# Kernel optimization log

Measured on AMD Instinct MI355X. Metric: run time of the kernel, lower is better.

## Reference

```python
import jax, jax.numpy as jnp
import numpy as np

B, N, D, H, PSI = 8, 7225, 256, 8, 64
DH = D // H
DF = 4 * D
EPS = 1e-5


def _ln(x, g, b):
    m = jnp.mean(x, axis=-1, keepdims=True)
    v = jnp.mean((x - m) ** 2, axis=-1, keepdims=True)
    return (x - m) / jnp.sqrt(v + EPS) * g + b


def _gelu(x):
    return jax.nn.gelu(x, approximate=False)


def setup_inputs() -> dict:
    key = jax.random.key(0)
    ks = jax.random.split(key, 16)
    w = lambda k, s: (jax.random.normal(k, s, dtype=jnp.float32) * 0.02)
    inp = {
        'x': jax.random.normal(ks[0], (B, N, D), dtype=jnp.float32),
        'fx': jax.random.normal(ks[1], (B, N, D), dtype=jnp.float32),
        'ln1_g': jnp.ones((D,), jnp.float32), 'ln1_b': jnp.zeros((D,), jnp.float32),
        'Wq': w(ks[2], (D, D)), 'Wk': w(ks[3], (D, D)), 'Wv': w(ks[4], (D, D)),
        'Wo': w(ks[5], (D, D)), 'bo': jnp.zeros((D,), jnp.float32),
        'ln2_g': jnp.ones((D,), jnp.float32), 'ln2_b': jnp.zeros((D,), jnp.float32),
        'mlp_W1': w(ks[6], (D, DF)), 'mlp_b1': jnp.zeros((DF,), jnp.float32),
        'mlp_W2': w(ks[7], (DF, D)), 'mlp_b2': jnp.zeros((D,), jnp.float32),
        'proj_W1': w(ks[8], (D, D)), 'proj_b1': jnp.zeros((D,), jnp.float32),
        'proj_W2': w(ks[9], (D, PSI)), 'proj_b2': jnp.zeros((PSI,), jnp.float32),
        'mu': jnp.zeros((PSI,), jnp.float32),
        'ln3_g': jnp.ones((D,), jnp.float32), 'ln3_b': jnp.zeros((D,), jnp.float32),
        'mlp2_W1': w(ks[10], (D, DF)), 'mlp2_b1': jnp.zeros((DF,), jnp.float32),
        'mlp2_W2': w(ks[11], (DF, D)), 'mlp2_b2': jnp.zeros((D,), jnp.float32),
    }
    return inp


def _forward(x, fx, ln1_g, ln1_b, Wq, Wk, Wv, Wo, bo, ln2_g, ln2_b,
             mlp_W1, mlp_b1, mlp_W2, mlp_b2, proj_W1, proj_b1, proj_W2, proj_b2,
             mu, ln3_g, ln3_b, mlp2_W1, mlp2_b1, mlp2_W2, mlp2_b2):
    # --- linear (kernelized, non-causal) self-attention ---
    h = _ln(x, ln1_g, ln1_b)
    to_heads = lambda t: t.reshape(B, N, H, DH).transpose(0, 2, 1, 3)  # bhnd
    q = to_heads(h @ Wq)
    k = to_heads(h @ Wk)
    v = to_heads(h @ Wv)
    q = jax.nn.softmax(q, axis=-1) * (DH ** -0.5)   # feature-dim softmax
    k = jax.nn.softmax(k, axis=-2)                  # sequence-dim softmax
    ctx = jnp.einsum('bhnd,bhne->bhde', k, v)       # [B,H,DH,DH]
    attn = jnp.einsum('bhnd,bhde->bhne', q, ctx)    # [B,H,N,DH]
    attn = attn.transpose(0, 2, 1, 3).reshape(B, N, D) @ Wo + bo
    x = attn + x

    # --- MLP block (n_layers=0, no residual inside MLP) ---
    h = _ln(x, ln2_g, ln2_b)
    x = _gelu(h @ mlp_W1 + mlp_b1) @ mlp_W2 + mlp_b2 + x

    # --- low-rank projection + covariance whitening (orth=True, training path) ---
    x_ = _gelu(x @ proj_W1 + proj_b1) @ proj_W2 + proj_b2       # [B,N,PSI]
    cov = jnp.einsum('blc,bld->cd', x_, x_) / (B * N)           # [PSI,PSI]
    L = jnp.linalg.cholesky(cov)
    L_inv_T = jnp.linalg.inv(L).T
    x_ = x_ @ L_inv_T

    # --- softplus-scaled low-rank operator on fx ---
    ctx2 = jnp.einsum('blp,bld->bpd', x_, fx)                   # [B,PSI,D]
    fx = jnp.einsum('blp,bpd->bld', x_ * jax.nn.softplus(mu), ctx2)

    fx = _gelu(_ln(fx, ln3_g, ln3_b) @ mlp2_W1 + mlp2_b1) @ mlp2_W2 + mlp2_b2
    return x, fx


def reference(x, fx, ln1_g, ln1_b, Wq, Wk, Wv, Wo, bo, ln2_g, ln2_b,
              mlp_W1, mlp_b1, mlp_W2, mlp_b2, proj_W1, proj_b1, proj_W2, proj_b2,
              mu, ln3_g, ln3_b, mlp2_W1, mlp2_b1, mlp2_W2, mlp2_b2):
    return _forward(x, fx, ln1_g, ln1_b, Wq, Wk, Wv, Wo, bo, ln2_g, ln2_b,
                    mlp_W1, mlp_b1, mlp_W2, mlp_b2, proj_W1, proj_b1, proj_W2, proj_b2,
                    mu, ln3_g, ln3_b, mlp2_W1, mlp2_b1, mlp2_W2, mlp2_b2)
```

## Files before the change

kernel.cpp:

```cpp
#include <hip/hip_runtime.h>
#include <math.h>

typedef unsigned short u16;
typedef unsigned int u32;
typedef float f32x4 __attribute__((ext_vector_type(4)));
typedef __bf16 bf16x8 __attribute__((ext_vector_type(8)));

#define NTOK 57800
#define NSEQ 7225
#define NBATCH 8

static __device__ __forceinline__ float bf2f(u16 u){ u32 x=((u32)u)<<16; float f; __builtin_memcpy(&f,&x,4); return f; }
static __device__ __forceinline__ u16 f2bf(float f){ u32 x; __builtin_memcpy(&x,&f,4); u32 r=x+0x7fffu+((x>>16)&1u); return (u16)(r>>16); }
static __device__ __forceinline__ float gelu_f(float v){
  float y = 0.7978845608028654f * v * (1.0f + 0.044715f * v * v);
  float ay = fabsf(y);
  float e = __expf(-2.0f * ay);
  float th = (1.0f - e) / (1.0f + e);
  th = (y < 0.f) ? -th : th;
  return 0.5f * v * (1.0f + th);
}

static __device__ __forceinline__ void gl16(const u16* g, u16* l){
  __builtin_amdgcn_global_load_lds((const __attribute__((address_space(1))) void*)g,
                                   (__attribute__((address_space(3))) void*)l, 16, 0, 0);
}

struct WJobs { const float* src[10]; u16* dst[10]; int K[10]; int N[10]; };
__global__ __launch_bounds__(256) void wtrans_all(WJobs j){
  int z = blockIdx.z;
  int K = j.K[z], N = j.N[z];
  int bk = blockIdx.x*32, bn = blockIdx.y*32;
  if (bk >= K || bn >= N) return;
  const float* src = j.src[z];
  u16* dst = j.dst[z];
  __shared__ float t[32][33];
  int tx = threadIdx.x&31, ty = threadIdx.x>>5;
  #pragma unroll
  for (int u=0;u<4;u++){
    int k = bk+ty+u*8, n = bn+tx;
    if (k<K && n<N) t[ty+u*8][tx] = src[(long)k*N+n];
  }
  __syncthreads();
  #pragma unroll
  for (int u=0;u<4;u++){
    int n = bn+ty+u*8, k = bk+tx;
    if (n<N && k<K) dst[(long)n*K+k] = f2bf(t[tx][ty+u*8]);
  }
}

__global__ __launch_bounds__(256) void ln_kernel(const float* __restrict__ in, const float* __restrict__ g,
                                                 const float* __restrict__ b, u16* __restrict__ out, int rows){
  int wid = threadIdx.x>>6, lane = threadIdx.x&63;
  int row = blockIdx.x*4 + wid;
  if (row >= rows) return;
  const float4 xv = *reinterpret_cast<const float4*>(in + (long)row*256 + lane*4);
  float s = xv.x+xv.y+xv.z+xv.w;
  float s2 = xv.x*xv.x+xv.y*xv.y+xv.z*xv.z+xv.w*xv.w;
  #pragma unroll
  for (int o=32;o;o>>=1){ s += __shfl_xor(s,o,64); s2 += __shfl_xor(s2,o,64); }
  float mean = s*(1.f/256.f);
  float var = fmaxf(s2*(1.f/256.f) - mean*mean, 0.f);
  float rstd = rsqrtf(var + 1e-5f);
  float4 gv = *reinterpret_cast<const float4*>(g + lane*4);
  float4 bv = *reinterpret_cast<const float4*>(b + lane*4);
  ushort4 o4;
  o4.x = f2bf((xv.x-mean)*rstd*gv.x + bv.x);
  o4.y = f2bf((xv.y-mean)*rstd*gv.y + bv.y);
  o4.z = f2bf((xv.z-mean)*rstd*gv.z + bv.z);
  o4.w = f2bf((xv.w-mean)*rstd*gv.w + bv.w);
  *reinterpret_cast<ushort4*>(out + (long)row*256 + lane*4) = o4;
}

template<bool BIASF, bool RESF, bool GELUF, bool OF32, bool OBF16>
__global__ __launch_bounds__(256) void gemm3(const u16* __restrict__ A, const u16* __restrict__ Bt,
    const float* __restrict__ bias, const float* __restrict__ resid,
    float* __restrict__ outF, u16* __restrict__ outB,
    int M, int N, int K, int gn, long aB, long bB, long cB)
{
  __shared__ __align__(16) u16 lds[2][8192];
  int nwg = gridDim.x, bid = blockIdx.x;
  int qx = nwg>>3, rx = nwg&7;
  int xcd = bid&7, lin = bid>>3;
  int swz = (xcd<rx)? (xcd*(qx+1)+lin) : (rx + xcd*qx + lin);
  int mi_ = swz/gn;
  int m0 = mi_*128, n0 = (swz - mi_*gn)*128;

  const u16* Ab  = A  + (long)blockIdx.z*aB;
  const u16* Btb = Bt + (long)blockIdx.z*bB;
  long coff = (long)blockIdx.z*cB;
  int tid = threadIdx.x, w = tid>>6, l = tid&63;
  int lr = l>>3;
  int csrc = (((l&7) ^ lr) << 3);
  int l15 = l&15, lq = l>>4;
  int wm = (w>>1)*64, wn = (w&1)*64;
  int sx = (l15&7)<<3;

  f32x4 acc[4][4];
  #pragma unroll
  for (int a=0;a<4;a++)
    #pragma unroll
    for (int b2=0;b2<4;b2++)
      #pragma unroll
      for (int r2=0;r2<4;r2++) acc[a][b2][r2]=0.f;

  int nt = K>>6;

  auto STAGE = [&](int k0){
    #pragma unroll
    for (int u=0;u<4;u++){
      int rr = w*32 + u*8;
      gl16(Ab  + (long)(m0+rr+lr)*K + k0 + csrc, &lds[0][0] + rr*64 + l*8);
      gl16(Btb + (long)(n0+rr+lr)*K + k0 + csrc, &lds[1][0] + rr*64 + l*8);
    }
  };

  STAGE(0);
  for (int t=0;;t++){
    __syncthreads();
    #pragma unroll
    for (int ks=0;ks<2;ks++){
      bf16x8 af[4], bfv[4];
      int ko = ks*32 + lq*8;
      #pragma unroll
      for (int mi=0;mi<4;mi++)
        af[mi]  = *reinterpret_cast<const bf16x8*>(&lds[0][0] + (wm+mi*16+l15)*64 + (ko ^ sx));
      #pragma unroll
      for (int ni=0;ni<4;ni++)
        bfv[ni] = *reinterpret_cast<const bf16x8*>(&lds[1][0] + (wn+ni*16+l15)*64 + (ko ^ sx));
      #pragma unroll
      for (int mi=0;mi<4;mi++)
        #pragma unroll
        for (int ni=0;ni<4;ni++)
          acc[mi][ni] = __builtin_amdgcn_mfma_f32_16x16x32_bf16(bfv[ni], af[mi], acc[mi][ni], 0,0,0);
    }
    if (t+1 == nt) break;
    __syncthreads();
    STAGE((t+1)<<6);
  }

  #pragma unroll
  for (int mi=0;mi<4;mi++){
    int row = m0 + wm + mi*16 + l15;
    if (row >= M) continue;
    #pragma unroll
    for (int ni=0;ni<4;ni++){
      int col0 = n0 + wn + ni*16 + lq*4;
      if (col0 >= N) continue;
      f32x4 v = acc[mi][ni];
      if (BIASF){
        const float4 bv = *reinterpret_cast<const float4*>(bias + col0);
        v[0]+=bv.x; v[1]+=bv.y; v[2]+=bv.z; v[3]+=bv.w;
      }
      long idx = (long)row*N + col0;
      if (RESF){
        const float4 rv = *reinterpret_cast<const float4*>(resid + coff + idx);
        v[0]+=rv.x; v[1]+=rv.y; v[2]+=rv.z; v[3]+=rv.w;
      }
      if (GELUF){
        #pragma unroll
        for (int r2=0;r2<4;r2++) v[r2] = gelu_f(v[r2]);
      }
      if (OF32){
        float4 o; o.x=v[0]; o.y=v[1]; o.z=v[2]; o.w=v[3];
        *reinterpret_cast<float4*>(outF + coff + idx) = o;
      }
      if (OBF16){
        ushort4 o; o.x=f2bf(v[0]); o.y=f2bf(v[1]); o.z=f2bf(v[2]); o.w=f2bf(v[3]);
        *reinterpret_cast<ushort4*>(outB + coff + idx) = o;
      }
    }
  }
}

__global__ __launch_bounds__(256) void ctx_part(const u16* __restrict__ qkvb, float* __restrict__ part,
                                                float* __restrict__ spart2){
  int ch = blockIdx.x, bh = blockIdx.y; int b = bh>>3, h = bh&7;
  __shared__ float ek[8][32], vl[8][32];
  int tid = threadIdx.x;
  int d = tid&31, eg = (tid>>5)*4;
  float acc[4] = {0.f,0.f,0.f,0.f};
  float ssum = 0.f;
  int n0 = ch*226; int n1 = n0+226; if (n1 > NSEQ) n1 = NSEQ;
  for (int nb=n0; nb<n1; nb+=8){
    #pragma unroll
    for (int u=0;u<2;u++){
      int idx = tid + u*256; int r = idx>>6, c = idx&63;
      int n = nb + r;
      if (c < 32) ek[r][c]    = (n<n1)? __expf(bf2f(qkvb[((long)(b*NSEQ+n))*768 + 256 + h*32 + c])) : 0.f;
      else        vl[r][c-32] = (n<n1)? bf2f(qkvb[((long)(b*NSEQ+n))*768 + 512 + h*32 + (c-32)]) : 0.f;
    }
    __syncthreads();
    #pragma unroll
    for (int r=0;r<8;r++){
      float kv = ek[r][d];
      ssum += kv;
      #pragma unroll
      for (int j=0;j<4;j++) acc[j] += kv * vl[r][eg+j];
    }
    __syncthreads();
  }
  #pragma unroll
  for (int j=0;j<4;j++) part[((long)(bh*32+ch))*1024 + d*32 + eg + j] = acc[j];
  if (tid < 32) spart2[(bh*32+ch)*32 + d] = ssum;
}
__global__ void ctx_red(const float* __restrict__ part, const float* __restrict__ spart2,
                        float* __restrict__ ctx){
  int bh = blockIdx.x;
  __shared__ float sinvl[32];
  int tid = threadIdx.x;
  if (tid < 32){
    float s=0.f;
    for (int ch=0;ch<32;ch++) s += spart2[(bh*32+ch)*32 + tid];
    sinvl[tid] = 1.0f/s;
  }
  __syncthreads();
  for (int idx=tid; idx<1024; idx+=256){
    float s=0.f;
    for (int ch=0;ch<32;ch++) s += part[((long)(bh*32+ch))*1024 + idx];
    ctx[(long)bh*1024 + idx] = s * sinvl[idx>>5];
  }
}

__global__ __launch_bounds__(256) void qsoftmax(const u16* __restrict__ qkvb, u16* __restrict__ qsb){
  int wid = threadIdx.x>>6, lane = threadIdx.x&63;
  int n = blockIdx.x*4 + wid;
  int b = blockIdx.y;
  if (n >= NSEQ) return;
  const ushort4 qv = *reinterpret_cast<const ushort4*>(qkvb + ((long)(b*NSEQ+n))*768 + lane*4);
  float e0 = __expf(bf2f(qv.x)), e1 = __expf(bf2f(qv.y)),
        e2 = __expf(bf2f(qv.z)), e3 = __expf(bf2f(qv.w));
  float s = e0+e1+e2+e3;
  s += __shfl_xor(s,1,64); s += __shfl_xor(s,2,64); s += __shfl_xor(s,4,64);
  float r = 0.17677669529663687f / s;
  ushort4 o; o.x=f2bf(e0*r); o.y=f2bf(e1*r); o.z=f2bf(e2*r); o.w=f2bf(e3*r);
  *reinterpret_cast<ushort4*>(qsb + ((long)(b*NSEQ+n))*256 + lane*4) = o;
}

__global__ __launch_bounds__(256) void ctx_wo(const float* __restrict__ ctx, const u16* __restrict__ wot,
                                              u16* __restrict__ w2bt){
  int jg = blockIdx.x, b = blockIdx.y;
  int j0 = jg*32;
  __shared__ u16 wol[32][256];
  int tid = threadIdx.x;
  {
    int r = tid>>3, c = (tid&7)*32;
    const uint4* src = reinterpret_cast<const uint4*>(wot + (j0+r)*256 + c);
    uint4* dst = reinterpret_cast<uint4*>(&wol[r][c]);
    dst[0]=src[0]; dst[1]=src[1]; dst[2]=src[2]; dst[3]=src[3];
  }
  int h = tid>>5, d = tid&31;
  float creg[32];
  {
    const float4* cp = reinterpret_cast<const float4*>(ctx + (long)(b*8+h)*1024 + d*32);
    #pragma unroll
    for (int u=0;u<8;u++){ float4 v = cp[u]; creg[u*4]=v.x; creg[u*4+1]=v.y; creg[u*4+2]=v.z; creg[u*4+3]=v.w; }
  }
  __syncthreads();
  for (int jj=0;jj<32;jj++){
    const uint4* wp = reinterpret_cast<const uint4*>(&wol[jj][h*32]);
    float acc = 0.f;
    #pragma unroll
    for (int u=0;u<4;u++){
      uint4 wv = wp[u];
      acc += bf2f((u16)(wv.x&0xffffu))*creg[u*8+0] + bf2f((u16)(wv.x>>16))*creg[u*8+1]
           + bf2f((u16)(wv.y&0xffffu))*creg[u*8+2] + bf2f((u16)(wv.y>>16))*creg[u*8+3]
           + bf2f((u16)(wv.z&0xffffu))*creg[u*8+4] + bf2f((u16)(wv.z>>16))*creg[u*8+5]
           + bf2f((u16)(wv.w&0xffffu))*creg[u*8+6] + bf2f((u16)(wv.w>>16))*creg[u*8+7];
    }
    w2bt[((long)b*256 + j0+jj)*256 + tid] = f2bf(acc);
  }
}

__global__ __launch_bounds__(256) void cov_part(const float* __restrict__ xu, float* __restrict__ part){
  int ch = blockIdx.x;
  __shared__ float xl[2][8][64];
  int tid = threadIdx.x;
  int i = tid&63, jg = (tid>>6)*16;
  int lrow = tid>>5, lcol = (tid&31)*2;
  float acc[16];
  #pragma unroll
  for (int j=0;j<16;j++) acc[j]=0.f;
  int n0 = ch*113;
  const int NT = 15;
  float2 xr2;
  auto LOAD = [&](int t){
    int n = n0 + t*8 + lrow;
    if (n < n0+113 && n < NTOK) xr2 = *reinterpret_cast<const float2*>(xu + (long)n*64 + lcol);
    else { xr2.x = 0.f; xr2.y = 0.f; }
  };
  LOAD(0);
  for (int t=0; t<NT; t++){
    int cur = t&1;
    xl[cur][lrow][lcol] = xr2.x; xl[cur][lrow][lcol+1] = xr2.y;
    __syncthreads();
    if (t+1 < NT) LOAD(t+1);
    #pragma unroll
    for (int r=0;r<8;r++){
      float xv = xl[cur][r][i];
      const float4* fb = reinterpret_cast<const float4*>(&xl[cur][r][jg]);
      float4 f0=fb[0], f1=fb[1], f2=fb[2], f3=fb[3];
      acc[0]+=xv*f0.x; acc[1]+=xv*f0.y; acc[2]+=xv*f0.z; acc[3]+=xv*f0.w;
      acc[4]+=xv*f1.x; acc[5]+=xv*f1.y; acc[6]+=xv*f1.z; acc[7]+=xv*f1.w;
      acc[8]+=xv*f2.x; acc[9]+=xv*f2.y; acc[10]+=xv*f2.z; acc[11]+=xv*f2.w;
      acc[12]+=xv*f3.x; acc[13]+=xv*f3.y; acc[14]+=xv*f3.z; acc[15]+=xv*f3.w;
    }
    __syncthreads();
  }
  #pragma unroll
  for (int j=0;j<16;j++) part[(long)ch*4096 + (jg+j)*64 + i] = acc[j];
}
__global__ void cov_red(const float* __restrict__ part, float* __restrict__ cov){
  __shared__ float red[4][64];
  int o = blockIdx.x*64 + (threadIdx.x&63);
  int sl = threadIdx.x>>6;
  float s=0.f;
  for (int ch=sl; ch<512; ch+=4) s += part[(long)ch*4096 + o];
  if (sl>0) red[sl][threadIdx.x&63] = s;
  __syncthreads();
  if (sl==0){
    s += red[1][threadIdx.x&63] + red[2][threadIdx.x&63] + red[3][threadIdx.x&63];
    cov[o] = s * (1.0f/57800.0f);
  }
}

__global__ void chol_inv(const float* __restrict__ cov, float* __restrict__ Linv){
  __shared__ float a[64][65];
  __shared__ float inv[64][65];
  int t = threadIdx.x;
  for (int j=0;j<64;j++) a[t][j] = cov[t*64+j];
  __syncthreads();
  for (int j=0;j<64;j++){
    if (t == j){
      float s = a[j][j];
      for (int k2=0;k2<j;k2++) s -= a[j][k2]*a[j][k2];
      a[j][j] = sqrtf(fmaxf(s, 1e-20f));
    }
    __syncthreads();
    if (t > j){
      float s = a[t][j];
      for (int k2=0;k2<j;k2++) s -= a[t][k2]*a[j][k2];
      a[t][j] = s / a[j][j];
    }
    __syncthreads();
  }
  int c = t;
  inv[c][c] = 1.0f / a[c][c];
  for (int i=c+1;i<64;i++){
    float s = 0.f;
    for (int k2=c;k2<i;k2++) s += a[i][k2]*inv[k2][c];
    inv[i][c] = -s / a[i][i];
  }
  __syncthreads();
  for (int i=0;i<64;i++) Linv[i*64+c] = (c<=i)? inv[i][c] : 0.f;
}

__global__ __launch_bounds__(256) void whiten(const float* __restrict__ xu, const float* __restrict__ Linv,
                                              const float* __restrict__ mu, u16* __restrict__ xw, u16* __restrict__ xws){
  __shared__ float Ll[64][65];
  int tid = threadIdx.x;
  for (int u=0; u<16; u++){ int idx = u*256+tid; Ll[idx>>6][idx&63] = Linv[idx]; }
  __syncthreads();
  int wid = tid>>6, lane = tid&63;
  float m = mu[lane];
  float sp = (m > 20.f)? m : log1pf(expf(m));
  for (int rr=0; rr<4; rr++){
    int row = blockIdx.x*16 + wid*4 + rr;
    if (row >= NTOK) continue;
    float xj = xu[(long)row*64 + lane];
    float s = 0.f;
    #pragma unroll
    for (int j=0;j<64;j++) s += __shfl(xj, j, 64) * Ll[lane][j];
    xw[(long)row*64+lane]  = f2bf(s);
    xws[(long)row*64+lane] = f2bf(s * sp);
  }
}

__global__ __launch_bounds__(256) void ctx2_part(const u16* __restrict__ xw, const float* __restrict__ fx,
                                                 float* __restrict__ part){
  int cg = blockIdx.x, ch = blockIdx.y, b = blockIdx.z;
  __shared__ float xwlf[2][8][64];
  __shared__ float fxl[2][8][64];
  int tid = threadIdx.x;
  int p = tid&63, jg = (tid>>6)*16;
  int c0 = cg*64;
  int lrow = tid>>5, lcol = (tid&31)*2;
  float acc[16];
  #pragma unroll
  for (int j=0;j<16;j++) acc[j]=0.f;
  int n0 = ch*226;
  const int NT = 29;
  float2 fxr; float xwr0, xwr1;
  auto LOAD = [&](int t){
    int n = n0 + t*8 + lrow;
    if (n < n0+226 && n < NSEQ){
      fxr = *reinterpret_cast<const float2*>(fx + ((long)b*NSEQ+n)*256 + c0 + lcol);
      u32 xv = *reinterpret_cast<const u32*>(xw + ((long)b*NSEQ+n)*64 + lcol);
      xwr0 = bf2f((u16)(xv&0xffffu)); xwr1 = bf2f((u16)(xv>>16));
    } else { fxr.x=0.f; fxr.y=0.f; xwr0=0.f; xwr1=0.f; }
  };
  LOAD(0);
  for (int t=0; t<NT; t++){
    int cur = t&1;
    xwlf[cur][lrow][lcol] = xwr0; xwlf[cur][lrow][lcol+1] = xwr1;
    fxl[cur][lrow][lcol] = fxr.x; fxl[cur][lrow][lcol+1] = fxr.y;
    __syncthreads();
    if (t+1 < NT) LOAD(t+1);
    #pragma unroll
    for (int r=0;r<8;r++){
      float xv = xwlf[cur][r][p];
      const float4* fb = reinterpret_cast<const float4*>(&fxl[cur][r][jg]);
      float4 f0=fb[0], f1=fb[1], f2=fb[2], f3=fb[3];
      acc[0]+=xv*f0.x; acc[1]+=xv*f0.y; acc[2]+=xv*f0.z; acc[3]+=xv*f0.w;
      acc[4]+=xv*f1.x; acc[5]+=xv*f1.y; acc[6]+=xv*f1.z; acc[7]+=xv*f1.w;
      acc[8]+=xv*f2.x; acc[9]+=xv*f2.y; acc[10]+=xv*f2.z; acc[11]+=xv*f2.w;
      acc[12]+=xv*f3.x; acc[13]+=xv*f3.y; acc[14]+=xv*f3.z; acc[15]+=xv*f3.w;
    }
    __syncthreads();
  }
  long base = ((long)(b*32+ch)*256 + c0 + jg)*64 + p;
  #pragma unroll
  for (int j=0;j<16;j++) part[base + (long)j*64] = acc[j];
}
__global__ void ctx2_red(const float* __restrict__ part, u16* __restrict__ c2t){
  int b = blockIdx.y;
  int idx0 = blockIdx.x*1024 + threadIdx.x;
  #pragma unroll
  for (int u=0;u<4;u++){
    int id = idx0 + u*256;
    float s=0.f;
    for (int ch=0;ch<32;ch++) s += part[(long)(b*32+ch)*16384 + id];
    c2t[(long)b*16384 + id] = f2bf(s);
  }
}

extern "C" void kernel_launch(void* const* d_in, const int* in_sizes, int n_in,
                              void* d_out, int out_size, void* d_ws, size_t ws_size,
                              hipStream_t stream)
{
  (void)in_sizes; (void)n_in; (void)out_size; (void)ws_size;
  const float* x     = (const float*)d_in[0];
  const float* fx    = (const float*)d_in[1];
  const float* ln1_g = (const float*)d_in[2];
  const float* ln1_b = (const float*)d_in[3];
  const float* Wq    = (const float*)d_in[4];
  const float* Wk    = (const float*)d_in[5];
  const float* Wv    = (const float*)d_in[6];
  const float* Wo    = (const float*)d_in[7];
  const float* bo    = (const float*)d_in[8];
  const float* ln2_g = (const float*)d_in[9];
  const float* ln2_b = (const float*)d_in[10];
  const float* mW1   = (const float*)d_in[11];
  const float* mb1   = (const float*)d_in[12];
  const float* mW2   = (const float*)d_in[13];
  const float* mb2   = (const float*)d_in[14];
  const float* pW1   = (const float*)d_in[15];
  const float* pb1   = (const float*)d_in[16];
  const float* pW2   = (const float*)d_in[17];
  const float* pb2   = (const float*)d_in[18];
  const float* mu    = (const float*)d_in[19];
  const float* ln3_g = (const float*)d_in[20];
  const float* ln3_b = (const float*)d_in[21];
  const float* m2W1  = (const float*)d_in[22];
  const float* m2b1  = (const float*)d_in[23];
  const float* m2W2  = (const float*)d_in[24];
  const float* m2b2  = (const float*)d_in[25];

  char* wsb = (char*)d_ws;
  u16* wt    = (u16*)wsb;
  u16* WQKVT = wt + 0;
  u16* WOT   = wt + 196608;
  u16* W1T   = wt + 262144;
  u16* W2T   = wt + 524288;
  u16* PW1T  = wt + 786432;
  u16* PW2T  = wt + 851968;
  u16* M2W1T = wt + 884736;
  u16* M2W2T = wt + 1146880;

  constexpr size_t OFF_H      = 2818048;
  constexpr size_t OFF_QKV    = 32440320;
  constexpr size_t OFF_ATT    = 150929408;
  constexpr size_t OFF_SPART2 = 180551680;
  constexpr size_t OFF_XU     = 180813824;
  constexpr size_t OFF_CTXP   = OFF_XU;
  constexpr size_t OFF_CTX    = OFF_XU + 8388608;
  constexpr size_t OFF_XW     = 195624960;
  constexpr size_t OFF_XWS    = 203023360;
  constexpr size_t OFF_W2BT   = 210430976;
  constexpr size_t OFF_COVP   = OFF_H;
  constexpr size_t OFF_COV    = OFF_H + 8388608;
  constexpr size_t OFF_LINV   = OFF_H + 8404992;
  constexpr size_t OFF_C2P    = OFF_QKV;
  constexpr size_t OFF_C2T    = OFF_QKV + 16777216;

  u16* h     = (u16*)(wsb + OFF_H);
  u16* qkvb  = (u16*)(wsb + OFF_QKV);
  u16* m1    = qkvb;
  u16* attb  = (u16*)(wsb + OFF_ATT);
  u16* qsb   = (u16*)(wsb + OFF_ATT);
  float* spart2= (float*)(wsb + OFF_SPART2);
  float* ctxp  = (float*)(wsb + OFF_CTXP);
  float* ctxb  = (float*)(wsb + OFF_CTX);
  float* xu    = (float*)(wsb + OFF_XU);
  u16*  xwb    = (u16*)(wsb + OFF_XW);
  u16*  xwsb   = (u16*)(wsb + OFF_XWS);
  float* covp  = (float*)(wsb + OFF_COVP);
  float* cov   = (float*)(wsb + OFF_COV);
  float* Linv  = (float*)(wsb + OFF_LINV);
  float* c2p   = (float*)(wsb + OFF_C2P);
  u16*  c2t    = (u16*)(wsb + OFF_C2T);
  u16*  w2bt   = (u16*)(wsb + OFF_W2BT);

  float* outx  = (float*)d_out;
  float* outfx = outx + 14796800;

  WJobs wj;
  wj.src[0]=Wq;   wj.dst[0]=WQKVT;          wj.K[0]=256;  wj.N[0]=256;
  wj.src[1]=Wk;   wj.dst[1]=WQKVT+65536;    wj.K[1]=256;  wj.N[1]=256;
  wj.src[2]=Wv;   wj.dst[2]=WQKVT+131072;   wj.K[2]=256;  wj.N[2]=256;
  wj.src[3]=Wo;   wj.dst[3]=WOT;            wj.K[3]=256;  wj.N[3]=256;
  wj.src[4]=mW1;  wj.dst[4]=W1T;            wj.K[4]=256;  wj.N[4]=1024;
  wj.src[5]=mW2;  wj.dst[5]=W2T;            wj.K[5]=1024; wj.N[5]=256;
  wj.src[6]=pW1;  wj.dst[6]=PW1T;           wj.K[6]=256;  wj.N[6]=256;
  wj.src[7]=pW2;  wj.dst[7]=PW2T;           wj.K[7]=256;  wj.N[7]=64;
  wj.src[8]=m2W1; wj.dst[8]=M2W1T;          wj.K[8]=256;  wj.N[8]=1024;
  wj.src[9]=m2W2; wj.dst[9]=M2W2T;          wj.K[9]=1024; wj.N[9]=256;
  wtrans_all<<<dim3(32,32,10),256,0,stream>>>(wj);

  ln_kernel<<<14450,256,0,stream>>>(x, ln1_g, ln1_b, h, NTOK);
  gemm3<false,false,false,false,true><<<dim3(452*6,1,1),256,0,stream>>>(
      h, WQKVT, nullptr, nullptr, nullptr, qkvb, NTOK, 768, 256, 6, 0,0,0);
  qsoftmax<<<dim3(1807,8),256,0,stream>>>(qkvb, qsb);
  ctx_part<<<dim3(32,64),256,0,stream>>>(qkvb, ctxp, spart2);
  ctx_red<<<64,256,0,stream>>>(ctxp, spart2, ctxb);
  ctx_wo<<<dim3(8,8),256,0,stream>>>(ctxb, WOT, w2bt);
  gemm3<true,true,false,true,false><<<dim3(57*2,1,8),256,0,stream>>>(
      qsb, w2bt, bo, x, outx, nullptr, NSEQ, 256, 256, 2,
      (long)NSEQ*256, 256*256, (long)NSEQ*256);

  ln_kernel<<<14450,256,0,stream>>>(outx, ln2_g, ln2_b, h, NTOK);
  gemm3<true,false,true,false,true><<<dim3(452*8,1,1),256,0,stream>>>(
      h, W1T, mb1, nullptr, nullptr, m1, NTOK, 1024, 256, 8, 0,0,0);
  gemm3<true,true,false,true,true><<<dim3(452*2,1,1),256,0,stream>>>(
      m1, W2T, mb2, outx, outx, attb, NTOK, 256, 1024, 2, 0,0,0);

  gemm3<true,false,true,false,true><<<dim3(452*2,1,1),256,0,stream>>>(
      attb, PW1T, pb1, nullptr, nullptr, h, NTOK, 256, 256, 2, 0,0,0);
  gemm3<true,false,false,true,false><<<dim3(452,1,1),256,0,stream>>>(
      h, PW2T, pb2, nullptr, xu, nullptr, NTOK, 64, 256, 1, 0,0,0);

  cov_part<<<512,256,0,stream>>>(xu, covp);
  cov_red<<<64,256,0,stream>>>(covp, cov);
  chol_inv<<<1,64,0,stream>>>(cov, Linv);
  whiten<<<3613,256,0,stream>>>(xu, Linv, mu, xwb, xwsb);

  ctx2_part<<<dim3(4,32,8),256,0,stream>>>(xwb, fx, c2p);
  ctx2_red<<<dim3(16,8),256,0,stream>>>(c2p, c2t);
  gemm3<false,false,false,true,false><<<dim3(57*2,1,8),256,0,stream>>>(
      xwsb, c2t, nullptr, nullptr, outfx, nullptr, NSEQ, 256, 64, 2,
      (long)NSEQ*64, 256*64, (long)NSEQ*256);

  ln_kernel<<<14450,256,0,stream>>>(outfx, ln3_g, ln3_b, h, NTOK);
  gemm3<true,false,true,false,true><<<dim3(452*8,1,1),256,0,stream>>>(
      h, M2W1T, m2b1, nullptr, nullptr, m1, NTOK, 1024, 256, 8, 0,0,0);
  gemm3<true,false,false,true,false><<<dim3(452*2,1,1),256,0,stream>>>(
      m1, M2W2T, m2b2, nullptr, outfx, nullptr, NTOK, 256, 1024, 2, 0,0,0);
}
```

Measured before the change: 904.9 us.

## Rewrite Cholesky inverse as single-wavefront register kernel using readlane broadcasts

```diff
diff --git a/kernel.cpp b/kernel.cpp
--- a/kernel.cpp
+++ b/kernel.cpp
@@ -24,6 +24,13 @@
 static __device__ __forceinline__ void gl16(const u16* g, u16* l){
   __builtin_amdgcn_global_load_lds((const __attribute__((address_space(1))) void*)g,
                                    (__attribute__((address_space(3))) void*)l, 16, 0, 0);
+}
+
+static __device__ __forceinline__ float rdlane(float v, int lane){
+  int i; __builtin_memcpy(&i,&v,4);
+  int r = __builtin_amdgcn_readlane(i, lane);
+  float f; __builtin_memcpy(&f,&r,4);
+  return f;
 }
 
 struct WJobs { const float* src[10]; u16* dst[10]; int K[10]; int N[10]; };
@@ -324,35 +331,41 @@
   }
 }
 
-__global__ void chol_inv(const float* __restrict__ cov, float* __restrict__ Linv){
-  __shared__ float a[64][65];
-  __shared__ float inv[64][65];
+__global__ __launch_bounds__(64) void chol_inv(const float* __restrict__ cov, float* __restrict__ Linv){
   int t = threadIdx.x;
-  for (int j=0;j<64;j++) a[t][j] = cov[t*64+j];
-  __syncthreads();
+  float r[64];
+  #pragma unroll
+  for (int k=0;k<16;k++){
+    float4 v4 = *reinterpret_cast<const float4*>(cov + (long)t*64 + k*4);
+    r[k*4]=v4.x; r[k*4+1]=v4.y; r[k*4+2]=v4.z; r[k*4+3]=v4.w;
+  }
+  float dinv[64];
+  #pragma unroll
   for (int j=0;j<64;j++){
-    if (t == j){
-      float s = a[j][j];
-      for (int k2=0;k2<j;k2++) s -= a[j][k2]*a[j][k2];
-      a[j][j] = sqrtf(fmaxf(s, 1e-20f));
-    }
-    __syncthreads();
-    if (t > j){
-      float s = a[t][j];
-      for (int k2=0;k2<j;k2++) s -= a[t][k2]*a[j][k2];
-      a[t][j] = s / a[j][j];
-    }
-    __syncthreads();
-  }
-  int c = t;
-  inv[c][c] = 1.0f / a[c][c];
-  for (int i=c+1;i<64;i++){
-    float s = 0.f;
-    for (int k2=c;k2<i;k2++) s += a[i][k2]*inv[k2][c];
-    inv[i][c] = -s / a[i][i];
-  }
-  __syncthreads();
-  for (int i=0;i<64;i++) Linv[i*64+c] = (c<=i)? inv[i][c] : 0.f;
+    float ajj = rdlane(r[j], j);
+    float ljj = sqrtf(fmaxf(ajj, 1e-20f));
+    float rinv = 1.0f / ljj;
+    dinv[j] = rinv;
+    float ltj = r[j] * rinv;
+    r[j] = ltj;
+    #pragma unroll
+    for (int k=j+1;k<64;k++){
+      float lkj = rdlane(ltj, k);
+      r[k] -= ltj * lkj;
+    }
+  }
+  float v[64];
+  #pragma unroll
+  for (int k=0;k<64;k++) v[k] = (k==t) ? 1.f : 0.f;
+  #pragma unroll
+  for (int i=0;i<64;i++){
+    float xi = v[i] * dinv[i];
+    Linv[i*64 + t] = xi;
+    #pragma unroll
+    for (int k=i+1;k<64;k++){
+      v[k] -= rdlane(r[i], k) * xi;
+    }
+  }
 }
 
 __global__ __launch_bounds__(256) void whiten(const float* __restrict__ xu, const float* __restrict__ Linv,
```

Result: faster. 864.1 us (-4.5%).
